# Performance work log

Measured on AMD Instinct MI355X. Metric: run time of the kernel, lower is better.

## Reference

```python
import jax, jax.numpy as jnp
import numpy as np

C = 256      # edge_width
H = 8        # num_heads
D = C // H   # dot dim per head
SCALE = D ** (-0.5)
LN_EPS = 1e-5


def layernorm(x, g, b):
    mu = jnp.mean(x, axis=-1, keepdims=True)
    var = jnp.mean(jnp.square(x - mu), axis=-1, keepdims=True)
    return (x - mu) * jax.lax.rsqrt(var + LN_EPS) * g + b


def setup_inputs() -> dict:
    key = jax.random.key(0)
    ks = jax.random.split(key, 12)
    B, N = 1, 160
    s = 0.02
    return {
        "e": jax.random.normal(ks[0], (B, N, N, C), jnp.float32),
        "mask": jnp.zeros((B, N, N, H), jnp.float32),
        "ln_g": jnp.ones((C,), jnp.float32),
        "ln_b": jnp.zeros((C,), jnp.float32),
        "Wqkv_in": jax.random.normal(ks[1], (C, 3 * C), jnp.float32) * s,
        "bqkv_in": jnp.zeros((3 * C,), jnp.float32),
        "Weg_in": jax.random.normal(ks[2], (C, 2 * H), jnp.float32) * s,
        "beg_in": jnp.zeros((2 * H,), jnp.float32),
        "Wqkv_out": jax.random.normal(ks[3], (C, 3 * C), jnp.float32) * s,
        "bqkv_out": jnp.zeros((3 * C,), jnp.float32),
        "Weg_out": jax.random.normal(ks[4], (C, 2 * H), jnp.float32) * s,
        "beg_out": jnp.zeros((2 * H,), jnp.float32),
        "Wo": jax.random.normal(ks[5], (2 * C, C), jnp.float32) * s,
        "bo": jnp.zeros((C,), jnp.float32),
    }


def reference(e, mask, ln_g, ln_b, Wqkv_in, bqkv_in, Weg_in, beg_in,
              Wqkv_out, bqkv_out, Weg_out, beg_out, Wo, bo):
    B, N, _, _ = e.shape
    e_ln = layernorm(e, ln_g, ln_b)

    def split_qkv(W, b):
        qkv = e_ln @ W + b                       # [B,N,N,3C]
        q, k, v = jnp.split(qkv, 3, axis=-1)
        shp = (B, N, N, D, H)                    # (dot_dim, heads) heads fastest
        return q.reshape(shp) * SCALE, k.reshape(shp), v.reshape(shp)

    # ---- incoming triangle attention ----
    Q_in, K_in, V_in = split_qkv(Wqkv_in, bqkv_in)
    eg_in = (e_ln @ Weg_in + beg_in)[:, :, None, :, :]   # [B,N,1,N,2H]
    E_in, G_in = jnp.split(eg_in, 2, axis=-1)            # each [B,N,1,N,H]
    mask_in = mask[:, :, None]                           # [B,N,1,N,H]
    H_in = jnp.einsum('bijdh,bjkdh->bijkh', Q_in, K_in) + E_in
    A_in = jax.nn.softmax(H_in + mask_in, axis=3) * jax.nn.sigmoid(G_in + mask_in)
    Va_in = jnp.einsum('bijkh,bjkdh->bijdh', A_in, V_in)

    # ---- outgoing triangle attention ----
    Q_out, K_out, V_out = split_qkv(Wqkv_out, bqkv_out)
    eg_out = (e_ln @ Weg_out + beg_out)[:, :, :, None, :]  # [B,N,N,1,2H]
    E_out, G_out = jnp.split(eg_out, 2, axis=-1)           # each [B,N,N,1,H]
    mask_out = mask[:, :, :, None]                         # [B,N,N,1,H]
    H_out = jnp.einsum('bijdh,bkjdh->bkijh', Q_out, K_out) + E_out
    A_out = jax.nn.softmax(H_out + mask_out, axis=1) * jax.nn.sigmoid(G_out + mask_out)
    Va_out = jnp.einsum('bkijh,bkjdh->bijdh', A_out, V_out)

    Va = jnp.concatenate([Va_in, Va_out], axis=-1).reshape(B, N, N, 2 * C)
    return Va @ Wo + bo
```

## Files before the change

### kernel.cpp

```cpp
#include <hip/hip_runtime.h>

#define NDIM 160
#define MROWS (NDIM*NDIM)
#define NC1 1600
#define QK_SCALE 0.17677669529663687f
#define PSW 168

typedef __attribute__((ext_vector_type(8))) short bhalf8;
typedef __attribute__((ext_vector_type(4))) short short4v;
typedef __attribute__((ext_vector_type(4))) unsigned short ushort4v;
typedef __attribute__((ext_vector_type(4))) float floatx4;

static __device__ __forceinline__ short f2bf(float f) {
  unsigned int u = __builtin_bit_cast(unsigned int, f);
  u = (u + 0x7FFFu + ((u >> 16) & 1u)) >> 16;
  return (short)(u & 0xFFFFu);
}
static __device__ __forceinline__ float bf2f(unsigned short u) {
  return __builtin_bit_cast(float, ((unsigned int)u) << 16);
}
static __device__ __forceinline__ void gload_lds16(const short* g, short* l) {
  __builtin_amdgcn_global_load_lds(
      (const __attribute__((address_space(1))) void*)g,
      (__attribute__((address_space(3))) void*)l, 16, 0, 0);
}

__global__ __launch_bounds__(256) void prep_kernel(
    const float* __restrict__ Wqkv_in, const float* __restrict__ bqkv_in,
    const float* __restrict__ Weg_in, const float* __restrict__ beg_in,
    const float* __restrict__ Wqkv_out, const float* __restrict__ bqkv_out,
    const float* __restrict__ Weg_out, const float* __restrict__ beg_out,
    const float* __restrict__ Wo,
    short* __restrict__ WcT, float* __restrict__ biasc, short* __restrict__ WoT) {
  int idx = blockIdx.x * 256 + threadIdx.x;
  if (idx < NC1 * 256) {
    int n = idx >> 8, k = idx & 255;
    float w = 0.f;
    if (n < 768)        { w = Wqkv_in[k*768 + n];          if (n < 256) w *= QK_SCALE; }
    else if (n < 1536)  { int cc = n - 768; w = Wqkv_out[k*768 + cc]; if (cc < 256) w *= QK_SCALE; }
    else if (n < 1552)  { w = Weg_in[k*16 + (n - 1536)]; }
    else if (n < 1568)  { w = Weg_out[k*16 + (n - 1552)]; }
    WcT[n*256 + k] = f2bf(w);
    if (k == 0) {
      float bb = 0.f;
      if (n < 768)        { bb = bqkv_in[n];           if (n < 256) bb *= QK_SCALE; }
      else if (n < 1536)  { int cc = n - 768; bb = bqkv_out[cc]; if (cc < 256) bb *= QK_SCALE; }
      else if (n < 1552)  bb = beg_in[n - 1536];
      else if (n < 1568)  bb = beg_out[n - 1552];
      biasc[n] = bb;
    }
  } else {
    int i2 = idx - NC1 * 256;
    int c = i2 >> 9, cc = i2 & 511;
    int ch = (cc & 31) * 16 + (cc >> 5);
    WoT[c*512 + cc] = f2bf(Wo[ch*256 + c]);
  }
}

__global__ __launch_bounds__(256) void ln_kernel(
    const float* __restrict__ e, const float* __restrict__ g,
    const float* __restrict__ b, short* __restrict__ eln) {
  int row = blockIdx.x * 4 + (threadIdx.x >> 6);
  int lane = threadIdx.x & 63;
  float4 x = ((const float4*)(e + row*256))[lane];
  float s = x.x + x.y + x.z + x.w;
#pragma unroll
  for (int o = 1; o < 64; o <<= 1) s += __shfl_xor(s, o, 64);
  float mu = s * (1.f/256.f);
  float dx0 = x.x - mu, dx1 = x.y - mu, dx2 = x.z - mu, dx3 = x.w - mu;
  float q = dx0*dx0 + dx1*dx1 + dx2*dx2 + dx3*dx3;
#pragma unroll
  for (int o = 1; o < 64; o <<= 1) q += __shfl_xor(q, o, 64);
  float rstd = rsqrtf(q * (1.f/256.f) + 1e-5f);
  float4 gg = ((const float4*)g)[lane];
  float4 bb = ((const float4*)b)[lane];
  short4v y;
  y[0] = f2bf(dx0 * rstd * gg.x + bb.x);
  y[1] = f2bf(dx1 * rstd * gg.y + bb.y);
  y[2] = f2bf(dx2 * rstd * gg.z + bb.z);
  y[3] = f2bf(dx3 * rstd * gg.w + bb.w);
  ((short4v*)(eln + row*256))[lane] = y;
}

template<int K>
static __device__ __forceinline__ void gemm128_mainloop(
    const short* __restrict__ A0, const short* __restrict__ B0,
    short* SMEM, floatx4 (&acc)[4][4]) {
  const int wave = threadIdx.x >> 6, lane = threadIdx.x & 63;
  const int lr = lane & 15, lg = lane >> 4;
  const int wr = wave >> 1, wc = wave & 1;
  const int srow = (lane >> 2);
  const int scol = (lane & 3) * 8;
  constexpr int NSTEP = K / 32;

  auto stage = [&](int bsel, int s) {
#pragma unroll
    for (int q = 0; q < 2; q++) {
      int rbase = wave*32 + q*16;
      const short* ga = A0 + (rbase + srow)*K + s*32 + scol;
      short* la = SMEM + bsel*4096 + rbase*32;
      gload_lds16(ga, la);
      const short* gb = B0 + (rbase + srow)*K + s*32 + scol;
      short* lb = SMEM + 8192 + bsel*4096 + rbase*32;
      gload_lds16(gb, lb);
    }
  };

  stage(0, 0);
  __syncthreads();
  int bsel = 0;
  for (int s = 0; s < NSTEP; s++) {
    if (s + 1 < NSTEP) stage(bsel ^ 1, s + 1);
    bhalf8 af[4], bf[4];
#pragma unroll
    for (int mi = 0; mi < 4; mi++)
      af[mi] = *(const bhalf8*)(SMEM + bsel*4096 + (wr*64 + mi*16 + lr)*32 + lg*8);
#pragma unroll
    for (int ni = 0; ni < 4; ni++)
      bf[ni] = *(const bhalf8*)(SMEM + 8192 + bsel*4096 + (wc*64 + ni*16 + lr)*32 + lg*8);
#pragma unroll
    for (int mi = 0; mi < 4; mi++)
#pragma unroll
      for (int ni = 0; ni < 4; ni++)
        acc[mi][ni] = __builtin_amdgcn_mfma_f32_16x16x32_bf16(af[mi], bf[ni], acc[mi][ni], 0, 0, 0);
    __syncthreads();
    bsel ^= 1;
  }
}

__global__ __launch_bounds__(256) void qkv_gemm128_kernel(
    const short* __restrict__ eln, const short* __restrict__ WcT,
    const float* __restrict__ biasc,
    short* __restrict__ Qin, short* __restrict__ Kin, short* __restrict__ Vin,
    short* __restrict__ Qout, short* __restrict__ Kout) {
  int nt = blockIdx.x, mt = blockIdx.y;
  int part = nt >> 1;
  int n0 = part*256 + (nt & 1)*128;
  int m0 = mt * 128;
  __shared__ short SMEM[16384];
  floatx4 acc[4][4] = {};
  gemm128_mainloop<256>(eln + (size_t)m0*256, WcT + (size_t)n0*256, SMEM, acc);

  int wave = threadIdx.x >> 6, lane = threadIdx.x & 63;
  int lr = lane & 15, lg = lane >> 4;
  int wr = wave >> 1, wc = wave & 1;
  short (*T)[264] = (short(*)[264])SMEM;
#pragma unroll
  for (int c = 0; c < 4; c++) {
    __syncthreads();
    if (wr == (c >> 1)) {
#pragma unroll
      for (int i = 0; i < 2; i++) {
        int mi = (c & 1)*2 + i;
#pragma unroll
        for (int ni = 0; ni < 4; ni++)
#pragma unroll
          for (int r = 0; r < 4; r++) {
            int mm = i*16 + lg*4 + r;
            int nn = wc*64 + ni*16 + lr;
            T[mm][nn] = f2bf(acc[mi][ni][r] + biasc[n0 + nn]);
          }
      }
    }
    __syncthreads();
    int m0h = m0 + c*32;
    int ai = m0h / 160, bj0 = m0h % 160;
    if (part == 2) {
      int c2 = threadIdx.x & 127, half = threadIdx.x >> 7;
      int pcol = (nt & 1)*128 + c2;
      int d = pcol >> 3, h = pcol & 7;
      short vals[16];
#pragma unroll
      for (int m = 0; m < 16; m++) vals[m] = T[half*16 + m][c2];
      short* dst = Vin + ((size_t)(ai*8 + h)*32 + d)*160 + bj0 + half*16;
#pragma unroll
      for (int q = 0; q < 2; q++) *(bhalf8*)(dst + q*8) = *(const bhalf8*)(vals + q*8);
    } else {
      int m = threadIdx.x >> 3, h = threadIdx.x & 7;
      int bj = bj0 + m;
      short vals[16];
#pragma unroll
      for (int dd = 0; dd < 16; dd++) vals[dd] = T[m][h + dd*8];
      int d0 = (nt & 1) * 16;
      short* dst;
      if (part == 0)      dst = Qin  + ((size_t)(bj*8 + h)*160 + ai)*32 + d0;
      else if (part == 1) dst = Kin  + ((size_t)(ai*8 + h)*160 + bj)*32 + d0;
      else if (part == 3) dst = Qout + ((size_t)(bj*8 + h)*160 + ai)*32 + d0;
      else                dst = Kout + ((size_t)(bj*8 + h)*160 + ai)*32 + d0;
#pragma unroll
      for (int q = 0; q < 2; q++) *(bhalf8*)(dst + q*8) = *(const bhalf8*)(vals + q*8);
    }
  }
}

__global__ __launch_bounds__(256) void voutEG_kernel(
    const short* __restrict__ eln, const short* __restrict__ WcT,
    const float* __restrict__ biasc,
    short* __restrict__ Vout,
    float* __restrict__ Ein, float* __restrict__ Gin,
    float* __restrict__ Eout, float* __restrict__ Gout) {
  int wave = threadIdx.x >> 6, lane = threadIdx.x & 63;
  int lr = lane & 15, lg = lane >> 4;
  __shared__ short T[32][264];

  if (blockIdx.x == 0) {
    int n2 = blockIdx.y / 5; int bn1 = (blockIdx.y % 5) * 32;
    int m0 = bn1*160 + n2;
    const short* a0p = eln + (m0 + lr*160) * 256;
    const short* a1p = eln + (m0 + (16 + lr)*160) * 256;
    int nb = 5 * 256;
    int wn = nb + wave * 64;
    const short* b0p = WcT + (wn + lr) * 256;
    floatx4 acc[2][4] = {};
    for (int kk = 0; kk < 256; kk += 32) {
      int ko = kk + lg*8;
      bhalf8 a0 = *(const bhalf8*)(a0p + ko);
      bhalf8 a1 = *(const bhalf8*)(a1p + ko);
#pragma unroll
      for (int f = 0; f < 4; f++) {
        bhalf8 b = *(const bhalf8*)(b0p + f*16*256 + ko);
        acc[0][f] = __builtin_amdgcn_mfma_f32_16x16x32_bf16(a0, b, acc[0][f], 0, 0, 0);
        acc[1][f] = __builtin_amdgcn_mfma_f32_16x16x32_bf16(a1, b, acc[1][f], 0, 0, 0);
      }
    }
#pragma unroll
    for (int i = 0; i < 2; i++)
#pragma unroll
      for (int f = 0; f < 4; f++)
#pragma unroll
        for (int r = 0; r < 4; r++) {
          int mm = i*16 + lg*4 + r;
          int nn = wave*64 + f*16 + lr;
          T[mm][nn] = f2bf(acc[i][f][r] + biasc[nb + nn]);
        }
    __syncthreads();
    int c = threadIdx.x, h = c & 7, d = c >> 3;
    short vals[32];
#pragma unroll
    for (int m = 0; m < 32; m++) vals[m] = T[m][c];
    short* dst = Vout + ((size_t)(n2*8 + h)*32 + d)*160 + bn1;
#pragma unroll
    for (int q = 0; q < 4; q++) *(bhalf8*)(dst + q*8) = *(const bhalf8*)(vals + q*8);
  } else {
    int m0 = blockIdx.y * 32;
    int wn = 1536 + wave * 16;
    const short* a0p = eln + (m0 + lr) * 256;
    const short* a1p = eln + (m0 + 16 + lr) * 256;
    const short* b0p = WcT + (wn + lr) * 256;
    floatx4 acc[2] = {};
    for (int kk = 0; kk < 256; kk += 32) {
      int ko = kk + lg*8;
      bhalf8 a0 = *(const bhalf8*)(a0p + ko);
      bhalf8 a1 = *(const bhalf8*)(a1p + ko);
      bhalf8 b  = *(const bhalf8*)(b0p + ko);
      acc[0] = __builtin_amdgcn_mfma_f32_16x16x32_bf16(a0, b, acc[0], 0, 0, 0);
      acc[1] = __builtin_amdgcn_mfma_f32_16x16x32_bf16(a1, b, acc[1], 0, 0, 0);
    }
    int n = wn + lr;
    if (n < 1568) {
      int t = n - 1536;
      float* dst = (t < 8) ? Ein : (t < 16) ? Gin : (t < 24) ? Eout : Gout;
#pragma unroll
      for (int i = 0; i < 2; i++)
#pragma unroll
        for (int r = 0; r < 4; r++) {
          int m = m0 + i*16 + lg*4 + r;
          dst[m*8 + (t & 7)] = acc[i][r] + biasc[n];
        }
    }
  }
}

__global__ __launch_bounds__(256) void ems_kernel(
    const float* __restrict__ Ein, const float* __restrict__ Gin,
    const float* __restrict__ Eout, const float* __restrict__ Gout,
    const float* __restrict__ mask,
    unsigned short* __restrict__ EMS, unsigned short* __restrict__ GSS) {
  int idx = blockIdx.x * 256 + threadIdx.x;
  if (idx >= 16 * 25600) return;
  int hb = idx / 25600;
  int rem = idx - hb * 25600;
  int i = rem / 160, k = rem - i * 160;
  int br = hb >> 3, h = hb & 7;
  int src = br ? ((k*160 + i)*8 + h) : ((i*160 + k)*8 + h);
  float ev = br ? Eout[src] : Ein[src];
  float gv = br ? Gout[src] : Gin[src];
  float mv = mask[src];
  EMS[idx] = (unsigned short)f2bf(ev + mv);
  GSS[idx] = (unsigned short)f2bf(1.f / (1.f + __expf(-(gv + mv))));
}

__global__ __launch_bounds__(256, 4) void attn_kernel(
    const short* __restrict__ Qin, const short* __restrict__ Kin, const short* __restrict__ Vin,
    const short* __restrict__ Qout, const short* __restrict__ Kout, const short* __restrict__ Vout,
    const unsigned short* __restrict__ EMS, const unsigned short* __restrict__ GSS,
    short* __restrict__ Va) {
  int wave = threadIdx.x >> 6, lane = threadIdx.x & 63;
  int g = blockIdx.x * 4 + wave;
  int pair = g % 5;
  int u = g / 5;
  int h = u & 7;
  int v = u >> 3;
  int br = v & 1;
  int j = v >> 1;
  int lr = lane & 15, lg = lane >> 4;
  const short* Qg = (br ? Qout : Qin) + (j*8 + h) * 5120;
  const short* Kg = (br ? Kout : Kin) + (j*8 + h) * 5120;
  const short* Vg = (br ? Vout : Vin) + (j*8 + h) * 5120;
  const unsigned short* EMh = EMS + (br*8 + h) * 25600;
  const unsigned short* GSh = GSS + (br*8 + h) * 25600;
  __shared__ short Ps[4][16][PSW];

  bhalf8 kf[10];
#pragma unroll
  for (int kt = 0; kt < 10; kt++)
    kf[kt] = *(const bhalf8*)(Kg + (kt*16 + lr)*32 + lg*8);

  const floatx4 zero = {0.f, 0.f, 0.f, 0.f};
  int hh = br*8 + h;
#pragma unroll
  for (int qi = 0; qi < 2; qi++) {
    int qt = pair*2 + qi;
    int i0 = qt*16;
    bhalf8 qf = *(const bhalf8*)(Qg + (i0 + lr)*32 + lg*8);
    int erow = (i0 + lr)*160;
    float sum = 0.f;
#pragma unroll
    for (int kt = 0; kt < 10; kt++) {
      ushort4v em = *(const ushort4v*)(EMh + erow + kt*16 + lg*4);
      floatx4 c0;
      c0[0] = bf2f(em[0]); c0[1] = bf2f(em[1]); c0[2] = bf2f(em[2]); c0[3] = bf2f(em[3]);
      floatx4 s = __builtin_amdgcn_mfma_f32_16x16x32_bf16(kf[kt], qf, c0, 0, 0, 0);
      ushort4v gs = *(const ushort4v*)(GSh + erow + kt*16 + lg*4);
      float p0 = __expf(s[0]), p1 = __expf(s[1]), p2 = __expf(s[2]), p3 = __expf(s[3]);
      sum += (p0 + p1) + (p2 + p3);
      short4v pk;
      pk[0] = f2bf(p0 * bf2f(gs[0]));
      pk[1] = f2bf(p1 * bf2f(gs[1]));
      pk[2] = f2bf(p2 * bf2f(gs[2]));
      pk[3] = f2bf(p3 * bf2f(gs[3]));
      *(short4v*)(&Ps[wave][lr][kt*16 + lg*4]) = pk;
    }
    sum += __shfl_xor(sum, 16, 64);
    sum += __shfl_xor(sum, 32, 64);
    float rs = 1.f / sum;
    floatx4 acc0 = zero, acc1 = zero;
#pragma unroll
    for (int kc = 0; kc < 5; kc++) {
      bhalf8 ap  = *(const bhalf8*)(&Ps[wave][lr][kc*32 + lg*8]);
      bhalf8 bv0 = *(const bhalf8*)(Vg + lr*160 + kc*32 + lg*8);
      bhalf8 bv1 = *(const bhalf8*)(Vg + (16 + lr)*160 + kc*32 + lg*8);
      acc0 = __builtin_amdgcn_mfma_f32_16x16x32_bf16(bv0, ap, acc0, 0, 0, 0);
      acc1 = __builtin_amdgcn_mfma_f32_16x16x32_bf16(bv1, ap, acc1, 0, 0, 0);
    }
    short* vp = Va + ((size_t)(i0 + lr)*160 + j)*512 + hh*32;
    short4v o0, o1;
#pragma unroll
    for (int r = 0; r < 4; r++) {
      o0[r] = f2bf(acc0[r] * rs);
      o1[r] = f2bf(acc1[r] * rs);
    }
    *(short4v*)(vp + lg*4) = o0;
    *(short4v*)(vp + 16 + lg*4) = o1;
  }
}

__global__ __launch_bounds__(256) void out_gemm128_kernel(
    const short* __restrict__ Va, const short* __restrict__ WoT,
    const float* __restrict__ bo, float* __restrict__ out) {
  int n0 = blockIdx.x * 128, m0 = blockIdx.y * 128;
  __shared__ short SMEM[16384];
  floatx4 acc[4][4] = {};
  gemm128_mainloop<512>(Va + (size_t)m0*512, WoT + (size_t)n0*512, SMEM, acc);
  int wave = threadIdx.x >> 6, lane = threadIdx.x & 63;
  int lr = lane & 15, lg = lane >> 4;
  int wr = wave >> 1, wc = wave & 1;
#pragma unroll
  for (int mi = 0; mi < 4; mi++)
#pragma unroll
    for (int ni = 0; ni < 4; ni++)
#pragma unroll
      for (int r = 0; r < 4; r++) {
        int m = m0 + wr*64 + mi*16 + lg*4 + r;
        int n = n0 + wc*64 + ni*16 + lr;
        out[(size_t)m*256 + n] = acc[mi][ni][r] + bo[n];
      }
}

extern "C" void kernel_launch(void* const* d_in, const int* in_sizes, int n_in,
                              void* d_out, int out_size, void* d_ws, size_t ws_size,
                              hipStream_t stream) {
  const float* e        = (const float*)d_in[0];
  const float* mask     = (const float*)d_in[1];
  const float* ln_g     = (const float*)d_in[2];
  const float* ln_b     = (const float*)d_in[3];
  const float* Wqkv_in  = (const float*)d_in[4];
  const float* bqkv_in  = (const float*)d_in[5];
  const float* Weg_in   = (const float*)d_in[6];
  const float* beg_in   = (const float*)d_in[7];
  const float* Wqkv_out = (const float*)d_in[8];
  const float* bqkv_out = (const float*)d_in[9];
  const float* Weg_out  = (const float*)d_in[10];
  const float* beg_out  = (const float*)d_in[11];
  const float* Wo       = (const float*)d_in[12];
  const float* bo       = (const float*)d_in[13];
  float* out = (float*)d_out;

  char* ws = (char*)d_ws;
  size_t off = 0;
  auto alloc = [&](size_t bytes) -> void* {
    void* p = ws + off;
    off += (bytes + 255) & ~(size_t)255;
    return p;
  };
  short* eln   = (short*)alloc((size_t)MROWS*256*2);
  short* WcT   = (short*)alloc((size_t)NC1*256*2);
  float* biasc = (float*)alloc((size_t)NC1*4);
  short* WoT   = (short*)alloc((size_t)256*512*2);
  short* Qin   = (short*)alloc((size_t)160*8*160*32*2);
  short* Kin   = (short*)alloc((size_t)160*8*160*32*2);
  short* Vin   = (short*)alloc((size_t)160*8*160*32*2);
  short* Qout  = (short*)alloc((size_t)160*8*160*32*2);
  short* Kout  = (short*)alloc((size_t)160*8*160*32*2);
  short* Vout  = (short*)alloc((size_t)160*8*160*32*2);
  float* Ein   = (float*)alloc((size_t)160*160*8*4);
  float* Gin   = (float*)alloc((size_t)160*160*8*4);
  float* Eout  = (float*)alloc((size_t)160*160*8*4);
  float* Gout  = (float*)alloc((size_t)160*160*8*4);
  unsigned short* EMS = (unsigned short*)alloc((size_t)16*25600*2);
  unsigned short* GSS = (unsigned short*)alloc((size_t)16*25600*2);
  short* Vabuf = (short*)alloc((size_t)MROWS*512*2);

  prep_kernel<<<2112, 256, 0, stream>>>(Wqkv_in, bqkv_in, Weg_in, beg_in,
                                        Wqkv_out, bqkv_out, Weg_out, beg_out,
                                        Wo, WcT, biasc, WoT);
  ln_kernel<<<6400, 256, 0, stream>>>(e, ln_g, ln_b, eln);
  qkv_gemm128_kernel<<<dim3(10, 200), 256, 0, stream>>>(eln, WcT, biasc,
      Qin, Kin, Vin, Qout, Kout);
  voutEG_kernel<<<dim3(2, 800), 256, 0, stream>>>(eln, WcT, biasc,
      Vout, Ein, Gin, Eout, Gout);
  ems_kernel<<<1600, 256, 0, stream>>>(Ein, Gin, Eout, Gout, mask, EMS, GSS);
  attn_kernel<<<3200, 256, 0, stream>>>(Qin, Kin, Vin, Qout, Kout, Vout,
      EMS, GSS, Vabuf);
  out_gemm128_kernel<<<dim3(2, 200), 256, 0, stream>>>(Vabuf, WoT, bo, out);
}
```

Before: 291.4 us.

## Fold Vout and E/G projections into tiled QKV GEMM and interleave E/G buffers

Widens the combined weight to 1664 columns so the Vout and E/G projections run inside the 128x128 LDS-tiled QKV GEMM, replacing the separate unstaged voutEG kernel. Vout is written row-major and a small transpose kernel rearranges it. The E-plus-mask and sigmoid gate buffers are interleaved so attention loads both with one 16-byte read. The grid order is swapped so the M tiles vary fastest, which improves weight reuse in cache. This adds an extra transpose pass and an extra workspace buffer, and the E/G tile computes 128 columns to use only 32.

After: 245.9 us. -15.6%, faster.

```diff
diff --git a/kernel.cpp b/kernel.cpp
--- a/kernel.cpp
+++ b/kernel.cpp
@@ -2,13 +2,13 @@
 
 #define NDIM 160
 #define MROWS (NDIM*NDIM)
-#define NC1 1600
+#define NC2 1664
 #define QK_SCALE 0.17677669529663687f
 #define PSW 168
 
 typedef __attribute__((ext_vector_type(8))) short bhalf8;
 typedef __attribute__((ext_vector_type(4))) short short4v;
-typedef __attribute__((ext_vector_type(4))) unsigned short ushort4v;
+typedef __attribute__((ext_vector_type(8))) unsigned short ushort8;
 typedef __attribute__((ext_vector_type(4))) float floatx4;
 
 static __device__ __forceinline__ short f2bf(float f) {
@@ -33,7 +33,7 @@
     const float* __restrict__ Wo,
     short* __restrict__ WcT, float* __restrict__ biasc, short* __restrict__ WoT) {
   int idx = blockIdx.x * 256 + threadIdx.x;
-  if (idx < NC1 * 256) {
+  if (idx < NC2 * 256) {
     int n = idx >> 8, k = idx & 255;
     float w = 0.f;
     if (n < 768)        { w = Wqkv_in[k*768 + n];          if (n < 256) w *= QK_SCALE; }
@@ -49,8 +49,8 @@
       else if (n < 1568)  bb = beg_out[n - 1552];
       biasc[n] = bb;
     }
-  } else {
-    int i2 = idx - NC1 * 256;
+  } else if (idx < NC2 * 256 + 256 * 512) {
+    int i2 = idx - NC2 * 256;
     int c = i2 >> 9, cc = i2 & 511;
     int ch = (cc & 31) * 16 + (cc >> 5);
     WoT[c*512 + cc] = f2bf(Wo[ch*256 + c]);
@@ -132,10 +132,12 @@
     const short* __restrict__ eln, const short* __restrict__ WcT,
     const float* __restrict__ biasc,
     short* __restrict__ Qin, short* __restrict__ Kin, short* __restrict__ Vin,
-    short* __restrict__ Qout, short* __restrict__ Kout) {
-  int nt = blockIdx.x, mt = blockIdx.y;
-  int part = nt >> 1;
-  int n0 = part*256 + (nt & 1)*128;
+    short* __restrict__ Qout, short* __restrict__ Kout, short* __restrict__ VoutRM,
+    float* __restrict__ Ein, float* __restrict__ Gin,
+    float* __restrict__ Eout, float* __restrict__ Gout) {
+  int mt = blockIdx.x, y = blockIdx.y;
+  int part = y >> 1;
+  int n0 = y * 128;
   int m0 = mt * 128;
   __shared__ short SMEM[16384];
   floatx4 acc[4][4] = {};
@@ -144,6 +146,26 @@
   int wave = threadIdx.x >> 6, lane = threadIdx.x & 63;
   int lr = lane & 15, lg = lane >> 4;
   int wr = wave >> 1, wc = wave & 1;
+
+  if (y == 12) {
+    if (wc == 0) {
+#pragma unroll
+      for (int mi = 0; mi < 4; mi++)
+#pragma unroll
+        for (int ni = 0; ni < 2; ni++)
+#pragma unroll
+          for (int r = 0; r < 4; r++) {
+            int nn = ni*16 + lr;
+            int n = 1536 + nn;
+            int m = m0 + wr*64 + mi*16 + lg*4 + r;
+            int t = nn;
+            float* dst = (t < 8) ? Ein : (t < 16) ? Gin : (t < 24) ? Eout : Gout;
+            dst[(size_t)m*8 + (t & 7)] = acc[mi][ni][r] + biasc[n];
+          }
+    }
+    return;
+  }
+
   short (*T)[264] = (short(*)[264])SMEM;
 #pragma unroll
   for (int c = 0; c < 4; c++) {
@@ -167,7 +189,7 @@
     int ai = m0h / 160, bj0 = m0h % 160;
     if (part == 2) {
       int c2 = threadIdx.x & 127, half = threadIdx.x >> 7;
-      int pcol = (nt & 1)*128 + c2;
+      int pcol = (y & 1)*128 + c2;
       int d = pcol >> 3, h = pcol & 7;
       short vals[16];
 #pragma unroll
@@ -181,93 +203,35 @@
       short vals[16];
 #pragma unroll
       for (int dd = 0; dd < 16; dd++) vals[dd] = T[m][h + dd*8];
-      int d0 = (nt & 1) * 16;
+      int d0 = (y & 1) * 16;
       short* dst;
-      if (part == 0)      dst = Qin  + ((size_t)(bj*8 + h)*160 + ai)*32 + d0;
-      else if (part == 1) dst = Kin  + ((size_t)(ai*8 + h)*160 + bj)*32 + d0;
-      else if (part == 3) dst = Qout + ((size_t)(bj*8 + h)*160 + ai)*32 + d0;
-      else                dst = Kout + ((size_t)(bj*8 + h)*160 + ai)*32 + d0;
+      if (part == 0)      dst = Qin    + ((size_t)(bj*8 + h)*160 + ai)*32 + d0;
+      else if (part == 1) dst = Kin    + ((size_t)(ai*8 + h)*160 + bj)*32 + d0;
+      else if (part == 3) dst = Qout   + ((size_t)(bj*8 + h)*160 + ai)*32 + d0;
+      else if (part == 4) dst = Kout   + ((size_t)(bj*8 + h)*160 + ai)*32 + d0;
+      else                dst = VoutRM + ((size_t)(bj*8 + h)*160 + ai)*32 + d0;
 #pragma unroll
       for (int q = 0; q < 2; q++) *(bhalf8*)(dst + q*8) = *(const bhalf8*)(vals + q*8);
     }
   }
 }
 
-__global__ __launch_bounds__(256) void voutEG_kernel(
-    const short* __restrict__ eln, const short* __restrict__ WcT,
-    const float* __restrict__ biasc,
-    short* __restrict__ Vout,
-    float* __restrict__ Ein, float* __restrict__ Gin,
-    float* __restrict__ Eout, float* __restrict__ Gout) {
-  int wave = threadIdx.x >> 6, lane = threadIdx.x & 63;
-  int lr = lane & 15, lg = lane >> 4;
-  __shared__ short T[32][264];
-
-  if (blockIdx.x == 0) {
-    int n2 = blockIdx.y / 5; int bn1 = (blockIdx.y % 5) * 32;
-    int m0 = bn1*160 + n2;
-    const short* a0p = eln + (m0 + lr*160) * 256;
-    const short* a1p = eln + (m0 + (16 + lr)*160) * 256;
-    int nb = 5 * 256;
-    int wn = nb + wave * 64;
-    const short* b0p = WcT + (wn + lr) * 256;
-    floatx4 acc[2][4] = {};
-    for (int kk = 0; kk < 256; kk += 32) {
-      int ko = kk + lg*8;
-      bhalf8 a0 = *(const bhalf8*)(a0p + ko);
-      bhalf8 a1 = *(const bhalf8*)(a1p + ko);
-#pragma unroll
-      for (int f = 0; f < 4; f++) {
-        bhalf8 b = *(const bhalf8*)(b0p + f*16*256 + ko);
-        acc[0][f] = __builtin_amdgcn_mfma_f32_16x16x32_bf16(a0, b, acc[0][f], 0, 0, 0);
-        acc[1][f] = __builtin_amdgcn_mfma_f32_16x16x32_bf16(a1, b, acc[1][f], 0, 0, 0);
-      }
-    }
-#pragma unroll
-    for (int i = 0; i < 2; i++)
-#pragma unroll
-      for (int f = 0; f < 4; f++)
-#pragma unroll
-        for (int r = 0; r < 4; r++) {
-          int mm = i*16 + lg*4 + r;
-          int nn = wave*64 + f*16 + lr;
-          T[mm][nn] = f2bf(acc[i][f][r] + biasc[nb + nn]);
-        }
-    __syncthreads();
-    int c = threadIdx.x, h = c & 7, d = c >> 3;
-    short vals[32];
-#pragma unroll
-    for (int m = 0; m < 32; m++) vals[m] = T[m][c];
-    short* dst = Vout + ((size_t)(n2*8 + h)*32 + d)*160 + bn1;
-#pragma unroll
-    for (int q = 0; q < 4; q++) *(bhalf8*)(dst + q*8) = *(const bhalf8*)(vals + q*8);
-  } else {
-    int m0 = blockIdx.y * 32;
-    int wn = 1536 + wave * 16;
-    const short* a0p = eln + (m0 + lr) * 256;
-    const short* a1p = eln + (m0 + 16 + lr) * 256;
-    const short* b0p = WcT + (wn + lr) * 256;
-    floatx4 acc[2] = {};
-    for (int kk = 0; kk < 256; kk += 32) {
-      int ko = kk + lg*8;
-      bhalf8 a0 = *(const bhalf8*)(a0p + ko);
-      bhalf8 a1 = *(const bhalf8*)(a1p + ko);
-      bhalf8 b  = *(const bhalf8*)(b0p + ko);
-      acc[0] = __builtin_amdgcn_mfma_f32_16x16x32_bf16(a0, b, acc[0], 0, 0, 0);
-      acc[1] = __builtin_amdgcn_mfma_f32_16x16x32_bf16(a1, b, acc[1], 0, 0, 0);
-    }
-    int n = wn + lr;
-    if (n < 1568) {
-      int t = n - 1536;
-      float* dst = (t < 8) ? Ein : (t < 16) ? Gin : (t < 24) ? Eout : Gout;
-#pragma unroll
-      for (int i = 0; i < 2; i++)
-#pragma unroll
-        for (int r = 0; r < 4; r++) {
-          int m = m0 + i*16 + lg*4 + r;
-          dst[m*8 + (t & 7)] = acc[i][r] + biasc[n];
-        }
-    }
+__global__ __launch_bounds__(256) void vtrans_kernel(
+    const short* __restrict__ VoutRM, short* __restrict__ Vout) {
+  int p = blockIdx.x;
+  const short* src = VoutRM + (size_t)p*5120;
+  short* dst = Vout + (size_t)p*5120;
+  __shared__ short Ts[32][164];
+  for (int c = threadIdx.x; c < 640; c += 256) {
+    int k = c >> 2, dq = c & 3;
+    bhalf8 v = *(const bhalf8*)(src + k*32 + dq*8);
+#pragma unroll
+    for (int q = 0; q < 8; q++) Ts[dq*8 + q][k] = v[q];
+  }
+  __syncthreads();
+  for (int c = threadIdx.x; c < 640; c += 256) {
+    int d = c / 20, kq = c % 20;
+    *(bhalf8*)(dst + d*160 + kq*8) = *(const bhalf8*)(&Ts[d][kq*8]);
   }
 }
 
@@ -275,7 +239,7 @@
     const float* __restrict__ Ein, const float* __restrict__ Gin,
     const float* __restrict__ Eout, const float* __restrict__ Gout,
     const float* __restrict__ mask,
-    unsigned short* __restrict__ EMS, unsigned short* __restrict__ GSS) {
+    unsigned short* __restrict__ EGp) {
   int idx = blockIdx.x * 256 + threadIdx.x;
   if (idx >= 16 * 25600) return;
   int hb = idx / 25600;
@@ -286,15 +250,15 @@
   float ev = br ? Eout[src] : Ein[src];
   float gv = br ? Gout[src] : Gin[src];
   float mv = mask[src];
-  EMS[idx] = (unsigned short)f2bf(ev + mv);
-  GSS[idx] = (unsigned short)f2bf(1.f / (1.f + __expf(-(gv + mv))));
+  size_t base = (((size_t)hb*160 + i)*40 + (k >> 2))*8 + (k & 3);
+  EGp[base]     = (unsigned short)f2bf(ev + mv);
+  EGp[base + 4] = (unsigned short)f2bf(1.f / (1.f + __expf(-(gv + mv))));
 }
 
 __global__ __launch_bounds__(256, 4) void attn_kernel(
     const short* __restrict__ Qin, const short* __restrict__ Kin, const short* __restrict__ Vin,
     const short* __restrict__ Qout, const short* __restrict__ Kout, const short* __restrict__ Vout,
-    const unsigned short* __restrict__ EMS, const unsigned short* __restrict__ GSS,
-    short* __restrict__ Va) {
+    const unsigned short* __restrict__ EGp, short* __restrict__ Va) {
   int wave = threadIdx.x >> 6, lane = threadIdx.x & 63;
   int g = blockIdx.x * 4 + wave;
   int pair = g % 5;
@@ -307,8 +271,7 @@
   const short* Qg = (br ? Qout : Qin) + (j*8 + h) * 5120;
   const short* Kg = (br ? Kout : Kin) + (j*8 + h) * 5120;
   const short* Vg = (br ? Vout : Vin) + (j*8 + h) * 5120;
-  const unsigned short* EMh = EMS + (br*8 + h) * 25600;
-  const unsigned short* GSh = GSS + (br*8 + h) * 25600;
+  const unsigned short* EGh = EGp + (size_t)(br*8 + h) * 160 * 320;
   __shared__ short Ps[4][16][PSW];
 
   bhalf8 kf[10];
@@ -323,22 +286,21 @@
     int qt = pair*2 + qi;
     int i0 = qt*16;
     bhalf8 qf = *(const bhalf8*)(Qg + (i0 + lr)*32 + lg*8);
-    int erow = (i0 + lr)*160;
+    int erow = (i0 + lr)*320;
     float sum = 0.f;
 #pragma unroll
     for (int kt = 0; kt < 10; kt++) {
-      ushort4v em = *(const ushort4v*)(EMh + erow + kt*16 + lg*4);
+      ushort8 eg = *(const ushort8*)(EGh + erow + (kt*4 + lg)*8);
       floatx4 c0;
-      c0[0] = bf2f(em[0]); c0[1] = bf2f(em[1]); c0[2] = bf2f(em[2]); c0[3] = bf2f(em[3]);
+      c0[0] = bf2f(eg[0]); c0[1] = bf2f(eg[1]); c0[2] = bf2f(eg[2]); c0[3] = bf2f(eg[3]);
       floatx4 s = __builtin_amdgcn_mfma_f32_16x16x32_bf16(kf[kt], qf, c0, 0, 0, 0);
-      ushort4v gs = *(const ushort4v*)(GSh + erow + kt*16 + lg*4);
       float p0 = __expf(s[0]), p1 = __expf(s[1]), p2 = __expf(s[2]), p3 = __expf(s[3]);
       sum += (p0 + p1) + (p2 + p3);
       short4v pk;
-      pk[0] = f2bf(p0 * bf2f(gs[0]));
-      pk[1] = f2bf(p1 * bf2f(gs[1]));
-      pk[2] = f2bf(p2 * bf2f(gs[2]));
-      pk[3] = f2bf(p3 * bf2f(gs[3]));
+      pk[0] = f2bf(p0 * bf2f(eg[4]));
+      pk[1] = f2bf(p1 * bf2f(eg[5]));
+      pk[2] = f2bf(p2 * bf2f(eg[6]));
+      pk[3] = f2bf(p3 * bf2f(eg[7]));
       *(short4v*)(&Ps[wave][lr][kt*16 + lg*4]) = pk;
     }
     sum += __shfl_xor(sum, 16, 64);
@@ -368,7 +330,7 @@
 __global__ __launch_bounds__(256) void out_gemm128_kernel(
     const short* __restrict__ Va, const short* __restrict__ WoT,
     const float* __restrict__ bo, float* __restrict__ out) {
-  int n0 = blockIdx.x * 128, m0 = blockIdx.y * 128;
+  int m0 = blockIdx.x * 128, n0 = blockIdx.y * 128;
   __shared__ short SMEM[16384];
   floatx4 acc[4][4] = {};
   gemm128_mainloop<512>(Va + (size_t)m0*512, WoT + (size_t)n0*512, SMEM, acc);
@@ -413,34 +375,33 @@
     off += (bytes + 255) & ~(size_t)255;
     return p;
   };
-  short* eln   = (short*)alloc((size_t)MROWS*256*2);
-  short* WcT   = (short*)alloc((size_t)NC1*256*2);
-  float* biasc = (float*)alloc((size_t)NC1*4);
-  short* WoT   = (short*)alloc((size_t)256*512*2);
-  short* Qin   = (short*)alloc((size_t)160*8*160*32*2);
-  short* Kin   = (short*)alloc((size_t)160*8*160*32*2);
-  short* Vin   = (short*)alloc((size_t)160*8*160*32*2);
-  short* Qout  = (short*)alloc((size_t)160*8*160*32*2);
-  short* Kout  = (short*)alloc((size_t)160*8*160*32*2);
-  short* Vout  = (short*)alloc((size_t)160*8*160*32*2);
-  float* Ein   = (float*)alloc((size_t)160*160*8*4);
-  float* Gin   = (float*)alloc((size_t)160*160*8*4);
-  float* Eout  = (float*)alloc((size_t)160*160*8*4);
-  float* Gout  = (float*)alloc((size_t)160*160*8*4);
-  unsigned short* EMS = (unsigned short*)alloc((size_t)16*25600*2);
-  unsigned short* GSS = (unsigned short*)alloc((size_t)16*25600*2);
-  short* Vabuf = (short*)alloc((size_t)MROWS*512*2);
-
-  prep_kernel<<<2112, 256, 0, stream>>>(Wqkv_in, bqkv_in, Weg_in, beg_in,
+  short* eln    = (short*)alloc((size_t)MROWS*256*2);
+  short* WcT    = (short*)alloc((size_t)NC2*256*2);
+  float* biasc  = (float*)alloc((size_t)NC2*4);
+  short* WoT    = (short*)alloc((size_t)256*512*2);
+  short* Qin    = (short*)alloc((size_t)160*8*160*32*2);
+  short* Kin    = (short*)alloc((size_t)160*8*160*32*2);
+  short* Vin    = (short*)alloc((size_t)160*8*160*32*2);
+  short* Qout   = (short*)alloc((size_t)160*8*160*32*2);
+  short* Kout   = (short*)alloc((size_t)160*8*160*32*2);
+  short* VoutRM = (short*)alloc((size_t)160*8*160*32*2);
+  short* Vout   = (short*)alloc((size_t)160*8*160*32*2);
+  float* Ein    = (float*)alloc((size_t)160*160*8*4);
+  float* Gin    = (float*)alloc((size_t)160*160*8*4);
+  float* Eout   = (float*)alloc((size_t)160*160*8*4);
+  float* Gout   = (float*)alloc((size_t)160*160*8*4);
+  unsigned short* EGp = (unsigned short*)alloc((size_t)16*160*320*2);
+  short* Vabuf  = (short*)alloc((size_t)MROWS*512*2);
+
+  prep_kernel<<<2178, 256, 0, stream>>>(Wqkv_in, bqkv_in, Weg_in, beg_in,
                                         Wqkv_out, bqkv_out, Weg_out, beg_out,
                                         Wo, WcT, biasc, WoT);
   ln_kernel<<<6400, 256, 0, stream>>>(e, ln_g, ln_b, eln);
-  qkv_gemm128_kernel<<<dim3(10, 200), 256, 0, stream>>>(eln, WcT, biasc,
-      Qin, Kin, Vin, Qout, Kout);
-  voutEG_kernel<<<dim3(2, 800), 256, 0, stream>>>(eln, WcT, biasc,
-      Vout, Ein, Gin, Eout, Gout);
-  ems_kernel<<<1600, 256, 0, stream>>>(Ein, Gin, Eout, Gout, mask, EMS, GSS);
+  qkv_gemm128_kernel<<<dim3(200, 13), 256, 0, stream>>>(eln, WcT, biasc,
+      Qin, Kin, Vin, Qout, Kout, VoutRM, Ein, Gin, Eout, Gout);
+  vtrans_kernel<<<1280, 256, 0, stream>>>(VoutRM, Vout);
+  ems_kernel<<<1600, 256, 0, stream>>>(Ein, Gin, Eout, Gout, mask, EGp);
   attn_kernel<<<3200, 256, 0, stream>>>(Qin, Kin, Vin, Qout, Kout, Vout,
-      EMS, GSS, Vabuf);
-  out_gemm128_kernel<<<dim3(2, 200), 256, 0, stream>>>(Vabuf, WoT, bo, out);
-}
+      EGp, Vabuf);
+  out_gemm128_kernel<<<dim3(200, 2), 256, 0, stream>>>(Vabuf, WoT, bo, out);
+}
```
